# Optimization experiments

Hardware: AMD Instinct MI355X
Metric: run time of the kernel (lower is better)

## Reference

```python
import jax, jax.numpy as jnp
import numpy as np


def setup_inputs() -> dict:
    key = jax.random.key(0)
    ks = jax.random.split(key, 13)
    B, T, D, H, E, C, S = 256, 64, 512, 512, 256, 6624, 26
    s = 0.05
    return {
        "batch_H": jax.random.normal(ks[0], (B, T, D), jnp.float32),
        "text": jax.random.randint(ks[1], (B, S), 0, C, jnp.int64),
        "W_i2h": jax.random.normal(ks[2], (H, D), jnp.float32) * s,
        "W_h2h": jax.random.normal(ks[3], (H, H), jnp.float32) * s,
        "b_h2h": jax.random.normal(ks[4], (H,), jnp.float32) * s,
        "w_score": jax.random.normal(ks[5], (H,), jnp.float32) * s,
        "W_ih": jax.random.normal(ks[6], (4 * H, D + E), jnp.float32) * s,
        "W_hh": jax.random.normal(ks[7], (4 * H, H), jnp.float32) * s,
        "b_ih": jax.random.normal(ks[8], (4 * H,), jnp.float32) * s,
        "b_hh": jax.random.normal(ks[9], (4 * H,), jnp.float32) * s,
        "emb": jax.random.normal(ks[10], (C, E), jnp.float32) * s,
        "W_gen": jax.random.normal(ks[11], (C, H), jnp.float32) * s,
        "b_gen": jax.random.normal(ks[12], (C,), jnp.float32) * s,
        "max_label_length": 25,
    }


def reference(batch_H, text, W_i2h, W_h2h, b_h2h, w_score, W_ih, W_hh,
              b_ih, b_hh, emb, W_gen, b_gen, max_label_length):
    B, T, D = batch_H.shape
    H = W_h2h.shape[0]
    num_steps = max_label_length + 1

    # i2h(batch_H) is constant across steps -> hoist out of the recurrence
    Hproj = jnp.einsum('btd,hd->bth', batch_H, W_i2h)  # [B,T,H]
    char_embs = emb[text[:, :num_steps]]               # [B,S,E]
    xs = jnp.transpose(char_embs, (1, 0, 2))           # [S,B,E]

    def step(carry, ce):
        h, c = carry
        hp = h @ W_h2h.T + b_h2h                       # [B,H]
        e = jnp.tanh(Hproj + hp[:, None, :]) @ w_score  # [B,T]
        alpha = jax.nn.softmax(e, axis=1)
        context = jnp.einsum('bt,btd->bd', alpha, batch_H)  # [B,D]
        x = jnp.concatenate([context, ce], axis=1)     # [B,D+E]
        gates = x @ W_ih.T + b_ih + h @ W_hh.T + b_hh  # [B,4H]
        i, f, g, o = jnp.split(gates, 4, axis=1)
        c_new = jax.nn.sigmoid(f) * c + jax.nn.sigmoid(i) * jnp.tanh(g)
        h_new = jax.nn.sigmoid(o) * jnp.tanh(c_new)
        return (h_new, c_new), h_new

    h0 = jnp.zeros((B, H), batch_H.dtype)
    c0 = jnp.zeros((B, H), batch_H.dtype)
    _, hs = jax.lax.scan(step, (h0, c0), xs)           # hs: [S,B,H]
    output_hiddens = jnp.transpose(hs, (1, 0, 2))      # [B,S,H]
    probs = output_hiddens @ W_gen.T + b_gen           # [B,S,C]
    return probs
```

## Files before the change

### kernel.cpp

```cpp
#include <hip/hip_runtime.h>

typedef unsigned short u16;
typedef unsigned int   u32;
typedef __attribute__((ext_vector_type(4))) float f32x4;
typedef __attribute__((ext_vector_type(8))) u16   u16x8;
typedef __attribute__((ext_vector_type(4))) u16   u16x4;
typedef __attribute__((ext_vector_type(4))) u32   u32x4;

__device__ __forceinline__ u16 f2bf(float x) {
  u32 u = __builtin_bit_cast(u32, x);
  u = (u + 0x7fffu + ((u >> 16) & 1u)) >> 16;
  return (u16)u;
}
__device__ __forceinline__ float bf2f(u16 h) {
  return __builtin_bit_cast(float, (u32)h << 16);
}
__device__ __forceinline__ float fast_sig(float x) { return 1.f / (1.f + __expf(-x)); }
__device__ __forceinline__ float fast_tanh(float x) {
  float e = __expf(2.f * x);
  return 1.f - 2.f / (e + 1.f);
}

__device__ __forceinline__ f32x4 mfma_bf16(u16x8 a, u16x8 b, f32x4 c) {
  asm volatile("v_mfma_f32_16x16x32_bf16 %0, %1, %2, %0" : "+v"(c) : "v"(a), "v"(b));
  return c;
}

__device__ __forceinline__ void gload_lds16(const void* g, void* l) {
  __builtin_amdgcn_global_load_lds(
      (__attribute__((address_space(1))) u32*)g,
      (__attribute__((address_space(3))) u32*)l, 16, 0, 0);
}

__device__ __forceinline__ void conv4(const float* __restrict__ s, u16* __restrict__ d, int i) {
  f32x4 v = *(const f32x4*)(s + i);
  u16x4 o;
  o.x = f2bf(v.x); o.y = f2bf(v.y); o.z = f2bf(v.z); o.w = f2bf(v.w);
  *(u16x4*)(d + i) = o;
}

__global__ __launch_bounds__(256) void k_prep(
    const float* __restrict__ batch_H, const float* __restrict__ W_i2h,
    const float* __restrict__ emb, const float* __restrict__ W_ih,
    const float* __restrict__ W_h2h, const float* __restrict__ W_hh,
    const float* __restrict__ W_gen, const float* __restrict__ b_ih,
    const float* __restrict__ b_hh, const float* __restrict__ b_h2h,
    u16* __restrict__ bHb, u16* __restrict__ Wi2hb, u16* __restrict__ embb,
    u16* __restrict__ Wctxb, u16* __restrict__ Wceb, u16* __restrict__ Whcatb,
    u16* __restrict__ Wgenb, float* __restrict__ biascat,
    u16* __restrict__ hb, float* __restrict__ cst,
    float* __restrict__ hpbuf, float* __restrict__ ghbuf) {
  const u32 u = blockIdx.x * 256 + threadIdx.x;
  if (u < 2097152u) { conv4(batch_H, bHb, u * 4); return; }
  if (u < 2162688u) { conv4(W_i2h, Wi2hb, (u - 2097152u) * 4); return; }
  if (u < 2586624u) { conv4(emb, embb, (u - 2162688u) * 4); return; }
  if (u < 2588672u) {
    *(u16x4*)(embb + 1695744u + (u - 2586624u) * 4) = (u16x4){0, 0, 0, 0};
    return;
  }
  if (u < 2850816u) {
    int i = (u - 2588672u) * 4;
    int r = i >> 9, c = i & 511;
    f32x4 v = *(const f32x4*)(W_ih + (size_t)r * 768 + c);
    u16x4 o;
    o.x = f2bf(v.x); o.y = f2bf(v.y); o.z = f2bf(v.z); o.w = f2bf(v.w);
    *(u16x4*)(Wctxb + i) = o;
    return;
  }
  if (u < 2981888u) {
    int i = (u - 2850816u) * 4;
    int r = i >> 8, c = i & 255;
    f32x4 v = *(const f32x4*)(W_ih + (size_t)r * 768 + 512 + c);
    u16x4 o;
    o.x = f2bf(v.x); o.y = f2bf(v.y); o.z = f2bf(v.z); o.w = f2bf(v.w);
    *(u16x4*)(Wceb + i) = o;
    return;
  }
  if (u < 3309568u) {
    int i = (u - 2981888u) * 4;
    int r = i >> 9, c = i & 511;
    const float* src = (r < 512) ? (W_h2h + (size_t)r * 512 + c)
                                 : (W_hh + (size_t)(r - 512) * 512 + c);
    f32x4 v = *(const f32x4*)src;
    u16x4 o;
    o.x = f2bf(v.x); o.y = f2bf(v.y); o.z = f2bf(v.z); o.w = f2bf(v.w);
    *(u16x4*)(Whcatb + i) = o;
    return;
  }
  if (u < 4161536u) {
    int i = (u - 3309568u) * 4;
    int r = i >> 9;
    if (r < 6624) conv4(W_gen, Wgenb, i);
    else *(u16x4*)(Wgenb + i) = (u16x4){0, 0, 0, 0};
    return;
  }
  if (u < 4162048u) {
    int j = (u - 4161536u) * 4;
    f32x4 a = *(const f32x4*)(b_ih + j), b = *(const f32x4*)(b_hh + j);
    f32x4 r = {a.x + b.x, a.y + b.y, a.z + b.z, a.w + b.w};
    *(f32x4*)(biascat + j) = r;
    return;
  }
  if (u < 4178432u) {
    *(u32x4*)((char*)hb + (size_t)(u - 4162048u) * 16) = (u32x4){0, 0, 0, 0};
    return;
  }
  if (u < 4211200u) {
    *(u32x4*)((char*)cst + (size_t)(u - 4178432u) * 16) = (u32x4){0, 0, 0, 0};
    return;
  }
  if (u < 4243968u) {
    int i = (u - 4211200u) * 4;
    int j = i & 511;
    *(f32x4*)(hpbuf + i) = *(const f32x4*)(b_h2h + j);
    return;
  }
  if (u < 4375040u) {
    *(u32x4*)((char*)ghbuf + (size_t)(u - 4243968u) * 16) = (u32x4){0, 0, 0, 0};
    return;
  }
}

template <int OUT_MODE>
__device__ __forceinline__ void gemm128_body(
    const u16* __restrict__ A, int lda, const u16* __restrict__ B, int ldb,
    const float* __restrict__ bias, float* __restrict__ Cf, u16* __restrict__ Cb,
    int ldc, int Nreal, int K, int m0, int n0, char* smem) {
  u16* sA = (u16*)smem;
  u16* sB = (u16*)(smem + 32768);
  const int tid = threadIdx.x;
  const int lane = tid & 63, wave = tid >> 6;
  const int wr = wave >> 1, wc = wave & 1;
  const int l15 = lane & 15, lhi = lane >> 4;

  f32x4 acc[4][4];
#pragma unroll
  for (int i = 0; i < 4; ++i)
#pragma unroll
    for (int j = 0; j < 4; ++j) acc[i][j] = 0.f;

  for (int k0 = 0; k0 < K; k0 += 128) {
    __syncthreads();
#pragma unroll
    for (int j = 0; j < 8; ++j) {
      int idx = j * 256 + tid, row = idx >> 4, cc = idx & 15, c = cc ^ (row & 15);
      gload_lds16(A + (size_t)(m0 + row) * lda + (k0 + c * 8), sA + idx * 8);
    }
#pragma unroll
    for (int j = 0; j < 8; ++j) {
      int idx = j * 256 + tid, row = idx >> 4, cc = idx & 15, c = cc ^ (row & 15);
      gload_lds16(B + (size_t)(n0 + row) * ldb + (k0 + c * 8), sB + idx * 8);
    }
    __syncthreads();

#pragma unroll
    for (int ks = 0; ks < 4; ++ks) {
      u16x8 av[4], bv[4];
#pragma unroll
      for (int mi = 0; mi < 4; ++mi) {
        int row = wr * 64 + mi * 16 + l15;
        int ch = row * 16 + ((ks * 4 + lhi) ^ (row & 15));
        av[mi] = *(const u16x8*)(sA + ch * 8);
      }
#pragma unroll
      for (int ni = 0; ni < 4; ++ni) {
        int row = wc * 64 + ni * 16 + l15;
        int ch = row * 16 + ((ks * 4 + lhi) ^ (row & 15));
        bv[ni] = *(const u16x8*)(sB + ch * 8);
      }
#pragma unroll
      for (int mi = 0; mi < 4; ++mi)
#pragma unroll
        for (int ni = 0; ni < 4; ++ni) acc[mi][ni] = mfma_bf16(av[mi], bv[ni], acc[mi][ni]);
    }
  }

  asm volatile("s_nop 7\ns_nop 7\ns_nop 7");

#pragma unroll
  for (int mi = 0; mi < 4; ++mi) {
#pragma unroll
    for (int ni = 0; ni < 4; ++ni) {
      int col = n0 + wc * 64 + ni * 16 + l15;
      if (col < Nreal) {
        float bvv = (OUT_MODE == 1) ? bias[col] : 0.f;
#pragma unroll
        for (int r = 0; r < 4; ++r) {
          int row = m0 + wr * 64 + mi * 16 + lhi * 4 + r;
          float v = acc[mi][ni][r] + bvv;
          if (OUT_MODE == 2)
            Cb[(size_t)row * ldc + col] = f2bf(v);
          else
            Cf[(size_t)row * ldc + col] = v;
        }
      }
    }
  }
}

template <int OUT_MODE>
__global__ __launch_bounds__(256) void kGemm128(const u16* __restrict__ A, int lda,
                                                const u16* __restrict__ B, int ldb,
                                                const float* __restrict__ bias,
                                                float* __restrict__ Cf, u16* __restrict__ Cb,
                                                int ldc, int Nreal, int K) {
  __shared__ __align__(16) char smem[65536];
  gemm128_body<OUT_MODE>(A, lda, B, ldb, bias, Cf, Cb, ldc, Nreal, K,
                         blockIdx.y * 128, blockIdx.x * 128, smem);
}

__global__ __launch_bounds__(256) void kHE(const u16* __restrict__ bHb,
                                           const u16* __restrict__ Wi2hb,
                                           u16* __restrict__ Hproj,
                                           const u16* __restrict__ embb,
                                           const u16* __restrict__ Wceb,
                                           const float* __restrict__ biascat,
                                           float* __restrict__ E2G) {
  __shared__ __align__(16) char smem[65536];
  const int bid = blockIdx.x;
  if (bid < 512) {
    gemm128_body<2>(bHb, 512, Wi2hb, 512, nullptr, nullptr, Hproj, 512, 512, 512,
                    (bid >> 2) * 128, (bid & 3) * 128, smem);
  } else {
    int r = bid - 512;
    gemm128_body<1>(embb, 256, Wceb, 256, biascat, E2G, nullptr, 2048, 2048, 256,
                    (r >> 4) * 128, (r & 15) * 128, smem);
  }
}

__device__ __forceinline__ void kA_body(int b0, int n0, const u16* __restrict__ hb,
                                        const u16* __restrict__ Whcatb,
                                        const float* __restrict__ b_h2h,
                                        float* __restrict__ hp, float* __restrict__ gh,
                                        char* smem) {
  u16* sA = (u16*)smem;
  u16* sB = (u16*)(smem + 8192);
  const int tid = threadIdx.x;
  const int lane = tid & 63, wave = tid >> 6;
  const int wr = wave >> 1, wc = wave & 1;
  const int l15 = lane & 15, lhi = lane >> 4;

  f32x4 acc[4];
#pragma unroll
  for (int j = 0; j < 4; ++j) acc[j] = 0.f;

  for (int k0 = 0; k0 < 512; k0 += 128) {
    __syncthreads();
#pragma unroll
    for (int j = 0; j < 2; ++j) {
      int idx = j * 256 + tid, row = idx >> 4, cc = idx & 15, c = cc ^ (row & 15);
      gload_lds16(hb + (size_t)(b0 + row) * 512 + k0 + c * 8, sA + idx * 8);
    }
#pragma unroll
    for (int j = 0; j < 8; ++j) {
      int idx = j * 256 + tid, row = idx >> 4, cc = idx & 15, c = cc ^ (row & 15);
      gload_lds16(Whcatb + (size_t)(n0 + row) * 512 + k0 + c * 8, sB + idx * 8);
    }
    __syncthreads();
#pragma unroll
    for (int ks = 0; ks < 4; ++ks) {
      u16x8 av, bv[4];
      {
        int row = wr * 16 + l15;
        int ch = row * 16 + ((ks * 4 + lhi) ^ (row & 15));
        av = *(const u16x8*)(sA + ch * 8);
      }
#pragma unroll
      for (int ni = 0; ni < 4; ++ni) {
        int row = wc * 64 + ni * 16 + l15;
        int ch = row * 16 + ((ks * 4 + lhi) ^ (row & 15));
        bv[ni] = *(const u16x8*)(sB + ch * 8);
      }
#pragma unroll
      for (int ni = 0; ni < 4; ++ni) acc[ni] = mfma_bf16(av, bv[ni], acc[ni]);
    }
  }
  asm volatile("s_nop 7\ns_nop 7\ns_nop 7");
#pragma unroll
  for (int ni = 0; ni < 4; ++ni) {
    int col = n0 + wc * 64 + ni * 16 + l15;
    int rowg = b0 + wr * 16 + lhi * 4;
    if (col < 512) {
      float bvv = b_h2h[col];
#pragma unroll
      for (int r = 0; r < 4; ++r)
        hp[(size_t)(rowg + r) * 512 + col] = acc[ni][r] + bvv;
    } else {
#pragma unroll
      for (int r = 0; r < 4; ++r)
        gh[(size_t)(rowg + r) * 2048 + col - 512] = acc[ni][r];
    }
  }
}

__global__ __launch_bounds__(256) void kA_hpgh(const u16* __restrict__ hb,
                                               const u16* __restrict__ Whcatb,
                                               const float* __restrict__ b_h2h,
                                               float* __restrict__ hpbuf,
                                               float* __restrict__ ghbuf) {
  __shared__ __align__(16) char smem[40960];
  kA_body(((int)blockIdx.x / 20) * 32, ((int)blockIdx.x % 20) * 128, hb, Whcatb, b_h2h,
          hpbuf, ghbuf, smem);
}

__global__ __launch_bounds__(256) void kAP(const u16* __restrict__ hb,
                                           const u16* __restrict__ Whcatb,
                                           const float* __restrict__ b_h2h,
                                           float* __restrict__ hpbuf,
                                           float* __restrict__ ghbuf,
                                           const u16* __restrict__ hsb,
                                           const u16* __restrict__ Wgenb,
                                           const float* __restrict__ b_gen,
                                           float* __restrict__ out, int sm1) {
  __shared__ __align__(16) char smem[65536];
  const int bid = blockIdx.x;
  if (bid < 160) {
    kA_body((bid / 20) * 32, (bid % 20) * 128, hb, Whcatb, b_h2h, hpbuf, ghbuf, smem);
  } else {
    int r = bid - 160;
    gemm128_body<1>(hsb + (size_t)sm1 * 512, 13312, Wgenb, 512, b_gen,
                    out + (size_t)sm1 * 6624, nullptr, 172224, 6624, 512,
                    (r / 52) * 128, (r % 52) * 128, smem);
  }
}

__global__ __launch_bounds__(256) void kB_attn(const u16* __restrict__ Hproj,
                                               const float* __restrict__ hpbuf,
                                               const float* __restrict__ wsc,
                                               const u16* __restrict__ bh,
                                               u16* __restrict__ ctxb) {
  const int b = blockIdx.x, tid = threadIdx.x;
  __shared__ float hpsp[528];
  __shared__ float wssp[528];
  __shared__ float es[64];

  {
    int j0 = tid * 2;
    hpsp[j0 + (j0 >> 5)] = hpbuf[(size_t)b * 512 + j0];
    hpsp[j0 + 1 + ((j0 + 1) >> 5)] = hpbuf[(size_t)b * 512 + j0 + 1];
    int pi = j0 + (j0 >> 5);
    wssp[pi] = wsc[j0];
    wssp[pi + 1] = wsc[j0 + 1];
  }
  __syncthreads();

  const int ch16 = tid & 15;
  const int hbase = ch16 * 33;
  const int hc = ch16 * 32;
  float hpr[32], wsr[32];
#pragma unroll
  for (int j = 0; j < 32; ++j) {
    hpr[j] = hpsp[hbase + j];
    wsr[j] = wssp[hbase + j];
  }
#pragma unroll
  for (int tg = 0; tg < 4; ++tg) {
    int t = tg * 16 + (tid >> 4);
    const u16* hr = Hproj + (size_t)(b * 64 + t) * 512 + hc;
    float s = 0.f;
#pragma unroll
    for (int jo = 0; jo < 32; jo += 8) {
      u16x8 hv = *(const u16x8*)(hr + jo);
#pragma unroll
      for (int j = 0; j < 8; ++j) {
        float x = bf2f(hv[j]) + hpr[jo + j];
        s += fast_tanh(x) * wsr[jo + j];
      }
    }
#pragma unroll
    for (int off = 8; off; off >>= 1) s += __shfl_xor(s, off, 16);
    if (ch16 == 0) es[t] = s;
  }
  __syncthreads();
  if (tid < 64) {
    float v = es[tid];
    float m = v;
#pragma unroll
    for (int o = 32; o; o >>= 1) m = fmaxf(m, __shfl_xor(m, o, 64));
    float p = __expf(v - m);
    float su = p;
#pragma unroll
    for (int o = 32; o; o >>= 1) su += __shfl_xor(su, o, 64);
    es[tid] = p / su;
  }
  __syncthreads();
  const u16* base = bh + (size_t)b * 32768 + tid * 2;
  float c0 = 0.f, c1 = 0.f;
#pragma unroll 8
  for (int t = 0; t < 64; ++t) {
    u32 w = *(const u32*)(base + t * 512);
    float a = es[t];
    c0 = fmaf(a, bf2f((u16)(w & 0xffffu)), c0);
    c1 = fmaf(a, bf2f((u16)(w >> 16)), c1);
  }
  u32 pk = (u32)f2bf(c0) | ((u32)f2bf(c1) << 16);
  *(u32*)(ctxb + (size_t)b * 512 + tid * 2) = pk;
}

__global__ __launch_bounds__(256) void kC_gates_lstm(const u16* __restrict__ ctxb,
                                                     const u16* __restrict__ Wctxb,
                                                     const float* __restrict__ E2G,
                                                     const float* __restrict__ ghbuf,
                                                     const int* __restrict__ text,
                                                     float* __restrict__ cst,
                                                     u16* __restrict__ hb,
                                                     u16* __restrict__ hsb, int step) {
  __shared__ __align__(16) char smem[40960];
  u16* sA = (u16*)smem;
  u16* sB = (u16*)(smem + 8192);
  const int tid = threadIdx.x;
  const int lane = tid & 63, wave = tid >> 6;
  const int wr = wave >> 1, wc = wave & 1;
  const int l15 = lane & 15, lhi = lane >> 4;
  const int jt = blockIdx.x;
  const int b0 = blockIdx.y * 32;

  f32x4 acc[4];
#pragma unroll
  for (int j = 0; j < 4; ++j) acc[j] = 0.f;

  for (int k0 = 0; k0 < 512; k0 += 128) {
    __syncthreads();
#pragma unroll
    for (int j = 0; j < 2; ++j) {
      int idx = j * 256 + tid, row = idx >> 4, cc = idx & 15, c = cc ^ (row & 15);
      gload_lds16(ctxb + (size_t)(b0 + row) * 512 + k0 + c * 8, sA + idx * 8);
    }
#pragma unroll
    for (int j = 0; j < 8; ++j) {
      int idx = j * 256 + tid, row = idx >> 4, cc = idx & 15, c = cc ^ (row & 15);
      int grow = (row >> 5) * 512 + jt * 32 + (row & 31);
      gload_lds16(Wctxb + (size_t)grow * 512 + k0 + c * 8, sB + idx * 8);
    }
    __syncthreads();

#pragma unroll
    for (int ks = 0; ks < 4; ++ks) {
      u16x8 av, bv[4];
      {
        int row = wr * 16 + l15;
        int ch = row * 16 + ((ks * 4 + lhi) ^ (row & 15));
        av = *(const u16x8*)(sA + ch * 8);
      }
#pragma unroll
      for (int ni = 0; ni < 4; ++ni) {
        int row = wc * 64 + ni * 16 + l15;
        int ch = row * 16 + ((ks * 4 + lhi) ^ (row & 15));
        bv[ni] = *(const u16x8*)(sB + ch * 8);
      }
#pragma unroll
      for (int ni = 0; ni < 4; ++ni) acc[ni] = mfma_bf16(av, bv[ni], acc[ni]);
    }
  }

  asm volatile("s_nop 7\ns_nop 7\ns_nop 7");
  __syncthreads();
  float (*gsm)[132] = (float(*)[132])smem;
#pragma unroll
  for (int ni = 0; ni < 4; ++ni) {
    int col = wc * 64 + ni * 16 + l15;
    int row = wr * 16 + lhi * 4;
#pragma unroll
    for (int r = 0; r < 4; ++r) gsm[row + r][col] = acc[ni][r];
  }
  __syncthreads();

  {
    const int bl = tid >> 3, jl0 = (tid & 7) * 4;
    const int b = b0 + bl;
    const int jg0 = jt * 32 + jl0;
    const int ci = text[b * 26 + step];
    const float* gh = ghbuf + (size_t)b * 2048;
    const float* ge = E2G + (size_t)ci * 2048;
    float cn[4];
    u16 hbv[4];
#pragma unroll
    for (int q = 0; q < 4; ++q) {
      int jl = jl0 + q, j = jg0 + q;
      float gi = gsm[bl][jl]      + gh[j]        + ge[j];
      float gf = gsm[bl][32 + jl] + gh[512 + j]  + ge[512 + j];
      float gg = gsm[bl][64 + jl] + gh[1024 + j] + ge[1024 + j];
      float go = gsm[bl][96 + jl] + gh[1536 + j] + ge[1536 + j];
      float c = fast_sig(gf) * cst[(size_t)b * 512 + j] + fast_sig(gi) * fast_tanh(gg);
      cn[q] = c;
      hbv[q] = f2bf(fast_sig(go) * fast_tanh(c));
    }
    *(f32x4*)(cst + (size_t)b * 512 + jg0) = *(f32x4*)cn;
    *(u16x4*)(hb + (size_t)b * 512 + jg0) = *(u16x4*)hbv;
    *(u16x4*)(hsb + (size_t)(b * 26 + step) * 512 + jg0) = *(u16x4*)hbv;
  }
}

extern "C" void kernel_launch(void* const* d_in, const int* in_sizes, int n_in,
                              void* d_out, int out_size, void* d_ws, size_t ws_size,
                              hipStream_t stream) {
  const float* batch_H = (const float*)d_in[0];
  const int*   text    = (const int*)d_in[1];
  const float* W_i2h   = (const float*)d_in[2];
  const float* W_h2h   = (const float*)d_in[3];
  const float* b_h2h   = (const float*)d_in[4];
  const float* w_score = (const float*)d_in[5];
  const float* W_ih    = (const float*)d_in[6];
  const float* W_hh    = (const float*)d_in[7];
  const float* b_ih    = (const float*)d_in[8];
  const float* b_hh    = (const float*)d_in[9];
  const float* emb     = (const float*)d_in[10];
  const float* W_gen   = (const float*)d_in[11];
  const float* b_gen   = (const float*)d_in[12];
  float* out = (float*)d_out;

  char* w0 = (char*)d_ws;
  char* w = w0;
  auto alloc = [&](size_t bytes) {
    char* p = w;
    w += (bytes + 255) & ~(size_t)255;
    return p;
  };
  u16*   Wi2hb   = (u16*)alloc(512ull * 512 * 2);
  u16*   Whcatb  = (u16*)alloc(2560ull * 512 * 2);
  u16*   Wctxb   = (u16*)alloc(2048ull * 512 * 2);
  u16*   Wceb    = (u16*)alloc(2048ull * 256 * 2);
  u16*   Wgenb   = (u16*)alloc(6656ull * 512 * 2);
  u16*   embb    = (u16*)alloc(6656ull * 256 * 2);
  float* biascat = (float*)alloc(2048ull * 4);
  u16*   ctxb    = (u16*)alloc(256ull * 512 * 2);
  u16*   hb      = (u16*)alloc(256ull * 512 * 2);
  float* cst     = (float*)alloc(256ull * 512 * 4);
  float* hpbuf   = (float*)alloc(256ull * 512 * 4);
  float* ghbuf   = (float*)alloc(256ull * 2048 * 4);
  u16*   hsb     = (u16*)alloc(6656ull * 512 * 2);
  float* E2G     = (float*)alloc(6656ull * 2048 * 4);

  size_t need = (size_t)(w - w0) + 2ull * 16777216 + 512;
  const bool inloop = ws_size >= need;
  u16* bHb;
  u16* Hproj;
  if (inloop) {
    bHb   = (u16*)alloc(8388608ull * 2);
    Hproj = (u16*)alloc(8388608ull * 2);
  } else {
    bHb   = (u16*)d_out;
    Hproj = bHb + 8388608;
  }

  k_prep<<<17090, 256, 0, stream>>>(batch_H, W_i2h, emb, W_ih, W_h2h, W_hh, W_gen,
                                    b_ih, b_hh, b_h2h, bHb, Wi2hb, embb, Wctxb, Wceb,
                                    Whcatb, Wgenb, biascat, hb, cst, hpbuf, ghbuf);

  kHE<<<1344, 256, 0, stream>>>(bHb, Wi2hb, Hproj, embb, Wceb, biascat, E2G);

  for (int s = 0; s < 26; ++s) {
    if (s > 0) {
      if (inloop)
        kAP<<<264, 256, 0, stream>>>(hb, Whcatb, b_h2h, hpbuf, ghbuf, hsb, Wgenb,
                                     b_gen, out, s - 1);
      else
        kA_hpgh<<<160, 256, 0, stream>>>(hb, Whcatb, b_h2h, hpbuf, ghbuf);
    }
    kB_attn<<<256, 256, 0, stream>>>(Hproj, hpbuf, w_score, bHb, ctxb);
    kC_gates_lstm<<<dim3(16, 8), 256, 0, stream>>>(ctxb, Wctxb, E2G, ghbuf, text,
                                                   cst, hb, hsb, s);
  }

  if (inloop) {
    kGemm128<1><<<dim3(52, 2), 256, 0, stream>>>(
        hsb + 25ull * 512, 13312, Wgenb, 512, b_gen, out + 25ull * 6624, nullptr,
        172224, 6624, 512);
  } else {
    kGemm128<1><<<dim3(52, 52), 256, 0, stream>>>(
        hsb, 512, Wgenb, 512, b_gen, out, nullptr, 6624, 6624, 512);
  }

  (void)in_sizes; (void)n_in; (void)out_size;
}
```

Baseline: 886.6 us.

## Drop per-step generator overlap; run one swizzled final output GEMM

Removes the in-loop path that fused the previous step's generator GEMM into the per-step hidden projection kernel. All 26 steps of output logits are now computed in a single 52x52-tile GEMM after the recurrence, with bHb/Hproj always aliased into the output buffer. Adds a block-index swizzle that spreads consecutive workgroups across the grid, aimed at cache locality. The trade is losing the overlap of generator work with the latency-bound recurrence in exchange for lighter per-step kernels and one large efficient GEMM.

```diff
diff --git a/kernel.cpp b/kernel.cpp
--- a/kernel.cpp
+++ b/kernel.cpp
@@ -198,15 +198,24 @@
   }
 }
 
-template <int OUT_MODE>
+template <int OUT_MODE, bool SWZ>
 __global__ __launch_bounds__(256) void kGemm128(const u16* __restrict__ A, int lda,
                                                 const u16* __restrict__ B, int ldb,
                                                 const float* __restrict__ bias,
                                                 float* __restrict__ Cf, u16* __restrict__ Cb,
                                                 int ldc, int Nreal, int K) {
   __shared__ __align__(16) char smem[65536];
+  int bx = blockIdx.x, by = blockIdx.y;
+  if (SWZ) {
+    int gx = gridDim.x;
+    int lin = by * gx + bx;
+    int q = (gx * gridDim.y) >> 3;
+    int idx = (lin & 7) * q + (lin >> 3);
+    by = idx / gx;
+    bx = idx - by * gx;
+  }
   gemm128_body<OUT_MODE>(A, lda, B, ldb, bias, Cf, Cb, ldc, Nreal, K,
-                         blockIdx.y * 128, blockIdx.x * 128, smem);
+                         by * 128, bx * 128, smem);
 }
 
 __global__ __launch_bounds__(256) void kHE(const u16* __restrict__ bHb,
@@ -228,17 +237,19 @@
   }
 }
 
-__device__ __forceinline__ void kA_body(int b0, int n0, const u16* __restrict__ hb,
-                                        const u16* __restrict__ Whcatb,
-                                        const float* __restrict__ b_h2h,
-                                        float* __restrict__ hp, float* __restrict__ gh,
-                                        char* smem) {
+__global__ __launch_bounds__(256) void kA_hpgh(const u16* __restrict__ hb,
+                                               const u16* __restrict__ Whcatb,
+                                               const float* __restrict__ b_h2h,
+                                               float* __restrict__ hpbuf,
+                                               float* __restrict__ ghbuf) {
+  __shared__ __align__(16) char smem[40960];
   u16* sA = (u16*)smem;
   u16* sB = (u16*)(smem + 8192);
   const int tid = threadIdx.x;
   const int lane = tid & 63, wave = tid >> 6;
   const int wr = wave >> 1, wc = wave & 1;
   const int l15 = lane & 15, lhi = lane >> 4;
+  const int b0 = ((int)blockIdx.x / 20) * 32, n0 = ((int)blockIdx.x % 20) * 128;
 
   f32x4 acc[4];
 #pragma unroll
@@ -284,43 +295,12 @@
       float bvv = b_h2h[col];
 #pragma unroll
       for (int r = 0; r < 4; ++r)
-        hp[(size_t)(rowg + r) * 512 + col] = acc[ni][r] + bvv;
+        hpbuf[(size_t)(rowg + r) * 512 + col] = acc[ni][r] + bvv;
     } else {
 #pragma unroll
       for (int r = 0; r < 4; ++r)
-        gh[(size_t)(rowg + r) * 2048 + col - 512] = acc[ni][r];
-    }
-  }
-}
-
-__global__ __launch_bounds__(256) void kA_hpgh(const u16* __restrict__ hb,
-                                               const u16* __restrict__ Whcatb,
-                                               const float* __restrict__ b_h2h,
-                                               float* __restrict__ hpbuf,
-                                               float* __restrict__ ghbuf) {
-  __shared__ __align__(16) char smem[40960];
-  kA_body(((int)blockIdx.x / 20) * 32, ((int)blockIdx.x % 20) * 128, hb, Whcatb, b_h2h,
-          hpbuf, ghbuf, smem);
-}
-
-__global__ __launch_bounds__(256) void kAP(const u16* __restrict__ hb,
-                                           const u16* __restrict__ Whcatb,
-                                           const float* __restrict__ b_h2h,
-                                           float* __restrict__ hpbuf,
-                                           float* __restrict__ ghbuf,
-                                           const u16* __restrict__ hsb,
-                                           const u16* __restrict__ Wgenb,
-                                           const float* __restrict__ b_gen,
-                                           float* __restrict__ out, int sm1) {
-  __shared__ __align__(16) char smem[65536];
-  const int bid = blockIdx.x;
-  if (bid < 160) {
-    kA_body((bid / 20) * 32, (bid % 20) * 128, hb, Whcatb, b_h2h, hpbuf, ghbuf, smem);
-  } else {
-    int r = bid - 160;
-    gemm128_body<1>(hsb + (size_t)sm1 * 512, 13312, Wgenb, 512, b_gen,
-                    out + (size_t)sm1 * 6624, nullptr, 172224, 6624, 512,
-                    (r / 52) * 128, (r % 52) * 128, smem);
+        ghbuf[(size_t)(rowg + r) * 2048 + col - 512] = acc[ni][r];
+    }
   }
 }
 
@@ -509,8 +489,10 @@
   const float* b_gen   = (const float*)d_in[12];
   float* out = (float*)d_out;
 
-  char* w0 = (char*)d_ws;
-  char* w = w0;
+  u16* bHb   = (u16*)d_out;
+  u16* Hproj = bHb + 8388608;
+
+  char* w = (char*)d_ws;
   auto alloc = [&](size_t bytes) {
     char* p = w;
     w += (bytes + 255) & ~(size_t)255;
@@ -531,18 +513,6 @@
   u16*   hsb     = (u16*)alloc(6656ull * 512 * 2);
   float* E2G     = (float*)alloc(6656ull * 2048 * 4);
 
-  size_t need = (size_t)(w - w0) + 2ull * 16777216 + 512;
-  const bool inloop = ws_size >= need;
-  u16* bHb;
-  u16* Hproj;
-  if (inloop) {
-    bHb   = (u16*)alloc(8388608ull * 2);
-    Hproj = (u16*)alloc(8388608ull * 2);
-  } else {
-    bHb   = (u16*)d_out;
-    Hproj = bHb + 8388608;
-  }
-
   k_prep<<<17090, 256, 0, stream>>>(batch_H, W_i2h, emb, W_ih, W_h2h, W_hh, W_gen,
                                     b_ih, b_hh, b_h2h, bHb, Wi2hb, embb, Wctxb, Wceb,
                                     Whcatb, Wgenb, biascat, hb, cst, hpbuf, ghbuf);
@@ -550,26 +520,14 @@
   kHE<<<1344, 256, 0, stream>>>(bHb, Wi2hb, Hproj, embb, Wceb, biascat, E2G);
 
   for (int s = 0; s < 26; ++s) {
-    if (s > 0) {
-      if (inloop)
-        kAP<<<264, 256, 0, stream>>>(hb, Whcatb, b_h2h, hpbuf, ghbuf, hsb, Wgenb,
-                                     b_gen, out, s - 1);
-      else
-        kA_hpgh<<<160, 256, 0, stream>>>(hb, Whcatb, b_h2h, hpbuf, ghbuf);
-    }
+    if (s > 0) kA_hpgh<<<160, 256, 0, stream>>>(hb, Whcatb, b_h2h, hpbuf, ghbuf);
     kB_attn<<<256, 256, 0, stream>>>(Hproj, hpbuf, w_score, bHb, ctxb);
     kC_gates_lstm<<<dim3(16, 8), 256, 0, stream>>>(ctxb, Wctxb, E2G, ghbuf, text,
                                                    cst, hb, hsb, s);
   }
 
-  if (inloop) {
-    kGemm128<1><<<dim3(52, 2), 256, 0, stream>>>(
-        hsb + 25ull * 512, 13312, Wgenb, 512, b_gen, out + 25ull * 6624, nullptr,
-        172224, 6624, 512);
-  } else {
-    kGemm128<1><<<dim3(52, 52), 256, 0, stream>>>(
-        hsb, 512, Wgenb, 512, b_gen, out, nullptr, 6624, 6624, 512);
-  }
-
-  (void)in_sizes; (void)n_in; (void)out_size;
-}
+  kGemm128<1, true><<<dim3(52, 52), 256, 0, stream>>>(
+      hsb, 512, Wgenb, 512, b_gen, out, nullptr, 6624, 6624, 512);
+
+  (void)in_sizes; (void)n_in; (void)out_size; (void)ws_size;
+}
```

Result: faster. 836.8 us (-5.6%).
